# Performance work log

Measured on AMD Instinct MI355X. Metric: run time of the kernel, lower is better.

The kernel has to match this reference:

```python
import jax, jax.numpy as jnp
import numpy as np

N_NODES = 4096
N_EDGES = 131072
C_IN = 256
C_OUT = 256
N_HEADS = 4
ALPHA = 0.2
NEG_FILL = -9e15


def setup_inputs() -> dict:
    key = jax.random.key(0)
    k_x, k_e, k_w, k_b, k_a = jax.random.split(key, 5)
    x = jax.random.normal(k_x, (N_NODES, C_IN), dtype=jnp.float32)
    edge_index = jax.random.randint(k_e, (2, N_EDGES), 0, N_NODES, dtype=jnp.int64)
    # nn.Linear(c_in, c_out): weight [c_out, c_in], bias [c_out]
    W = jax.random.normal(k_w, (C_OUT, C_IN), dtype=jnp.float32) * 0.05
    b = jax.random.normal(k_b, (C_OUT,), dtype=jnp.float32) * 0.05
    # attention vector a: [num_heads, 2 * c_out_per_head]
    a = jax.random.normal(k_a, (N_HEADS, 2 * (C_OUT // N_HEADS)), dtype=jnp.float32) * 0.05
    return {"x": x, "edge_index": edge_index, "W": W, "b": b, "a": a}


def reference(x, edge_index, W, b, a):
    N = x.shape[0]
    H = a.shape[0]
    C = W.shape[0] // H  # per-head feature dim

    # Linear projection then split heads: [N, H, C]
    feats = (x @ W.T + b).reshape(N, H, C)

    # Dense adjacency (faithful to the original index_select/scatter construction)
    adj = jnp.zeros((N, N), dtype=bool).at[edge_index[0], edge_index[1]].set(True)

    # attn_logits = leaky_relu(einsum('bhc,hc->bh', cat(f_i, f_j), a))
    # is separable: score(i,j,h) = leaky_relu(f_i . a[:, :C] + f_j . a[:, C:])
    s_src = jnp.einsum('nhc,hc->nh', feats, a[:, :C])  # [N, H]
    s_dst = jnp.einsum('nhc,hc->nh', feats, a[:, C:])  # [N, H]
    logits = jax.nn.leaky_relu(s_src[:, None, :] + s_dst[None, :, :], ALPHA)  # [N, N, H]

    masked = jnp.where(adj[..., None], logits, NEG_FILL)
    probs = jax.nn.softmax(masked, axis=1)  # softmax over source nodes j (dim=2 with batch)

    # Weighted aggregation: einsum('bijh,bjhc->bihc') then concat heads
    out = jnp.einsum('ijh,jhc->ihc', probs, feats).reshape(N, H * C)
    return out[None]  # [1, N, c_out] (batch_size = 1 in the original)
```

## Files before the change

### kernel.cpp

```cpp
#include <hip/hip_runtime.h>
#include <hip/hip_bf16.h>
#include <stdint.h>

#define N_NODES 4096
#define N_EDGES 131072
#define C_IN 256
#define C_OUT 256
#define N_HEADS 4
#define C_HEAD 64
#define MAX_DEG 128
#define GEMM_BLOCKS 1024
#define SCAT_BLOCKS 128

typedef __attribute__((ext_vector_type(8))) short short8;
typedef __attribute__((ext_vector_type(4))) short short4v;
typedef __attribute__((ext_vector_type(4))) float floatx4;

union f32u { float f; uint32_t u; };
__device__ __forceinline__ float bf2f(short s) {
    f32u v; v.u = ((uint32_t)(uint16_t)s) << 16; return v.f;
}
__device__ __forceinline__ short f2bf(float f) {
    __hip_bfloat16 h = __float2bfloat16(f);
    return *reinterpret_cast<short*>(&h);
}

__global__ __launch_bounds__(256) void k1_gemm_scatter(
    const float* __restrict__ x, const float* __restrict__ W,
    const float* __restrict__ b, const int* __restrict__ ei,
    unsigned short* __restrict__ nbr, int* __restrict__ deg,
    __hip_bfloat16* __restrict__ feats)
{
    int blk = blockIdx.x;
    int tid = threadIdx.x;
    if (blk < GEMM_BLOCKS) {
        int lane = tid & 63;
        int wave = tid >> 6;
        int tile = blk * 4 + wave;
        int row0 = (tile >> 4) * 16;
        int col0 = (tile & 15) * 16;
        int r    = lane & 15;
        int quad = lane >> 4;

        const floatx4* ax = (const floatx4*)(x + (size_t)(row0 + r) * C_IN);
        const floatx4* bw = (const floatx4*)(W + (size_t)(col0 + r) * C_IN);

        floatx4 acc = {0.f, 0.f, 0.f, 0.f};
        #pragma unroll
        for (int k8 = 0; k8 < 8; ++k8) {
            floatx4 a0 = ax[k8 * 8 + quad * 2], a1 = ax[k8 * 8 + quad * 2 + 1];
            floatx4 b0 = bw[k8 * 8 + quad * 2], b1 = bw[k8 * 8 + quad * 2 + 1];
            short8 av, bq;
            #pragma unroll
            for (int j = 0; j < 4; ++j) {
                av[j] = f2bf(a0[j]); av[4 + j] = f2bf(a1[j]);
                bq[j] = f2bf(b0[j]); bq[4 + j] = f2bf(b1[j]);
            }
            acc = __builtin_amdgcn_mfma_f32_16x16x32_bf16(av, bq, acc, 0, 0, 0);
        }
        int gn = col0 + r;
        float bias = b[gn];
        #pragma unroll
        for (int rr = 0; rr < 4; ++rr) {
            int gm = row0 + quad * 4 + rr;
            feats[(size_t)gm * C_OUT + gn] = __float2bfloat16(acc[rr] + bias);
        }
    } else {
        bool is64 = true;
        #pragma unroll
        for (int q = 1; q < 64; q += 2) is64 = is64 && (ei[q] == 0);
        int base = (blk - GEMM_BLOCKS) * 256 + tid;
        #pragma unroll
        for (int qq = 0; qq < 4; ++qq) {
            int e = base + qq * (SCAT_BLOCKS * 256);
            int row, col;
            if (is64) {
                const long long* e64 = (const long long*)ei;
                row = (int)e64[e];
                col = (int)e64[N_EDGES + e];
            } else {
                row = ei[e];
                col = ei[N_EDGES + e];
            }
            int pos = atomicAdd(&deg[row], 1);
            if (pos < MAX_DEG) nbr[row * MAX_DEG + pos] = (unsigned short)col;
        }
    }
}

__global__ __launch_bounds__(256) void aggregate(
    const unsigned short* __restrict__ nbr,
    const int* __restrict__ deg,
    const __hip_bfloat16* __restrict__ feats,
    const float* __restrict__ a,
    float* __restrict__ out)
{
    int i    = blockIdx.x;
    int t    = threadIdx.x;
    int wv   = t >> 6;
    int lane = t & 63;
    int h    = lane >> 4;
    int li   = lane & 15;

    __shared__ unsigned short lst[MAX_DEG];
    __shared__ unsigned char  ok[MAX_DEG];
    __shared__ uint32_t       bmap[N_NODES / 32];
    __shared__ float          ssrc_sh[N_HEADS];
    __shared__ floatx4        redv[4][64];
    __shared__ float          redd[4][64];

    int n = deg[i];
    n = (n < MAX_DEG) ? n : MAX_DEG;

    if (t < n) lst[t] = nbr[i * MAX_DEG + t];
    if (t < N_NODES / 32) bmap[t] = 0u;
    __syncthreads();

    if (t < n) {
        int j = lst[t];
        uint32_t bit = 1u << (j & 31);
        uint32_t old = atomicOr(&bmap[j >> 5], bit);
        ok[t] = (old & bit) ? 0 : 1;
    }

    floatx4 as4 = *(const floatx4*)(a + h * 2 * C_HEAD + 4 * li);
    floatx4 ad4 = *(const floatx4*)(a + h * 2 * C_HEAD + C_HEAD + 4 * li);

    if (wv == 0) {
        short4v fi = *(const short4v*)(feats + (size_t)i * C_OUT + lane * 4);
        float p = bf2f(fi[0]) * as4[0] + bf2f(fi[1]) * as4[1]
                + bf2f(fi[2]) * as4[2] + bf2f(fi[3]) * as4[3];
        p += __shfl_xor(p, 1, 16);
        p += __shfl_xor(p, 2, 16);
        p += __shfl_xor(p, 4, 16);
        p += __shfl_xor(p, 8, 16);
        if (li == 0) ssrc_sh[h] = p;
    }
    __syncthreads();

    float ssrc = ssrc_sh[h];
    floatx4 acc = {0.f, 0.f, 0.f, 0.f};
    float   den = 0.f;

    if (n > 0) {
        #pragma unroll 2
        for (int k = wv; k < n; k += 4) {
            int j = lst[k];
            short4v fv = *(const short4v*)(feats + (size_t)j * C_OUT + lane * 4);
            float f0 = bf2f(fv[0]), f1 = bf2f(fv[1]), f2 = bf2f(fv[2]), f3 = bf2f(fv[3]);
            float p = f0 * ad4[0] + f1 * ad4[1] + f2 * ad4[2] + f3 * ad4[3];
            p += __shfl_xor(p, 1, 16);
            p += __shfl_xor(p, 2, 16);
            p += __shfl_xor(p, 4, 16);
            p += __shfl_xor(p, 8, 16);
            float l = ssrc + p;
            l = (l > 0.f) ? l : 0.2f * l;
            float w = ok[k] ? __expf(fminf(l, 60.f)) : 0.f;
            den += w;
            acc[0] += w * f0; acc[1] += w * f1; acc[2] += w * f2; acc[3] += w * f3;
        }
    } else {
        for (int j = wv; j < N_NODES; j += 4) {
            short4v fv = *(const short4v*)(feats + (size_t)j * C_OUT + lane * 4);
            acc[0] += bf2f(fv[0]); acc[1] += bf2f(fv[1]);
            acc[2] += bf2f(fv[2]); acc[3] += bf2f(fv[3]);
            den += 1.0f;
        }
    }
    redv[wv][lane] = acc;
    redd[wv][lane] = den;
    __syncthreads();

    if (wv == 0) {
        floatx4 r0 = redv[0][lane], r1 = redv[1][lane], r2 = redv[2][lane], r3 = redv[3][lane];
        float d = redd[0][lane] + redd[1][lane] + redd[2][lane] + redd[3][lane];
        if (d <= 0.f) d = 1.f;
        float inv = 1.0f / d;
        floatx4 o;
        o[0] = (r0[0] + r1[0] + r2[0] + r3[0]) * inv;
        o[1] = (r0[1] + r1[1] + r2[1] + r3[1]) * inv;
        o[2] = (r0[2] + r1[2] + r2[2] + r3[2]) * inv;
        o[3] = (r0[3] + r1[3] + r2[3] + r3[3]) * inv;
        *(floatx4*)(out + (size_t)i * C_OUT + lane * 4) = o;
    }
}

extern "C" void kernel_launch(void* const* d_in, const int* in_sizes, int n_in,
                              void* d_out, int out_size, void* d_ws, size_t ws_size,
                              hipStream_t stream) {
    const float* x  = (const float*)d_in[0];
    const int*   ei = (const int*)d_in[1];
    const float* W  = (const float*)d_in[2];
    const float* b  = (const float*)d_in[3];
    const float* a  = (const float*)d_in[4];
    float* out = (float*)d_out;

    uint8_t* ws = (uint8_t*)d_ws;
    __hip_bfloat16* feats = (__hip_bfloat16*)ws;
    unsigned short* nbr   = (unsigned short*)(ws + (2u << 20));
    int*            deg   = (int*)(ws + (3u << 20));

    hipMemsetAsync(deg, 0, N_NODES * sizeof(int), stream);
    k1_gemm_scatter<<<GEMM_BLOCKS + SCAT_BLOCKS, 256, 0, stream>>>(x, W, b, ei, nbr, deg, feats);
    aggregate<<<N_NODES, 256, 0, stream>>>(nbr, deg, feats, a, out);
}
```

Baseline: 102.3 us.

## Precompute per-node attention scores in GEMM epilogue and cache edge weights in LDS

The GEMM epilogue now computes the per-head source and destination attention dot products from the fp32 projection. It reduces them across 16 lanes with shuffles and accumulates them into global ssrc/sdst arrays with atomics. The aggregate kernel then computes all edge weights once per neighbor in a prologue into shared memory, so the main gather loop only loads features and does the weighted sum without per-edge shuffles and exp. This removes redundant per-edge dot products and shuffle reductions, at the cost of extra atomics in the GEMM and a larger memset.

```diff
diff --git a/kernel.cpp b/kernel.cpp
--- a/kernel.cpp
+++ b/kernel.cpp
@@ -27,9 +27,11 @@
 
 __global__ __launch_bounds__(256) void k1_gemm_scatter(
     const float* __restrict__ x, const float* __restrict__ W,
-    const float* __restrict__ b, const int* __restrict__ ei,
+    const float* __restrict__ b, const float* __restrict__ a,
+    const int* __restrict__ ei,
     unsigned short* __restrict__ nbr, int* __restrict__ deg,
-    __hip_bfloat16* __restrict__ feats)
+    __hip_bfloat16* __restrict__ feats,
+    float* __restrict__ ssrc_g, float* __restrict__ sdst_g)
 {
     int blk = blockIdx.x;
     int tid = threadIdx.x;
@@ -59,11 +61,25 @@
             acc = __builtin_amdgcn_mfma_f32_16x16x32_bf16(av, bq, acc, 0, 0, 0);
         }
         int gn = col0 + r;
+        int h  = col0 >> 6;
         float bias = b[gn];
+        float avs = a[h * 2 * C_HEAD + (gn & 63)];
+        float avd = a[h * 2 * C_HEAD + C_HEAD + (gn & 63)];
         #pragma unroll
         for (int rr = 0; rr < 4; ++rr) {
             int gm = row0 + quad * 4 + rr;
-            feats[(size_t)gm * C_OUT + gn] = __float2bfloat16(acc[rr] + bias);
+            float v = acc[rr] + bias;
+            feats[(size_t)gm * C_OUT + gn] = __float2bfloat16(v);
+            float s = v * avs;
+            float d = v * avd;
+            s += __shfl_xor(s, 1, 16); s += __shfl_xor(s, 2, 16);
+            s += __shfl_xor(s, 4, 16); s += __shfl_xor(s, 8, 16);
+            d += __shfl_xor(d, 1, 16); d += __shfl_xor(d, 2, 16);
+            d += __shfl_xor(d, 4, 16); d += __shfl_xor(d, 8, 16);
+            if (r == 0) {
+                atomicAdd(&ssrc_g[gm * N_HEADS + h], s);
+                atomicAdd(&sdst_g[gm * N_HEADS + h], d);
+            }
         }
     } else {
         bool is64 = true;
@@ -92,7 +108,8 @@
     const unsigned short* __restrict__ nbr,
     const int* __restrict__ deg,
     const __hip_bfloat16* __restrict__ feats,
-    const float* __restrict__ a,
+    const float* __restrict__ ssrc_g,
+    const float* __restrict__ sdst_g,
     float* __restrict__ out)
 {
     int i    = blockIdx.x;
@@ -100,12 +117,10 @@
     int wv   = t >> 6;
     int lane = t & 63;
     int h    = lane >> 4;
-    int li   = lane & 15;
 
     __shared__ unsigned short lst[MAX_DEG];
-    __shared__ unsigned char  ok[MAX_DEG];
+    __shared__ floatx4        wts4[MAX_DEG];
     __shared__ uint32_t       bmap[N_NODES / 32];
-    __shared__ float          ssrc_sh[N_HEADS];
     __shared__ floatx4        redv[4][64];
     __shared__ float          redd[4][64];
 
@@ -120,44 +135,33 @@
         int j = lst[t];
         uint32_t bit = 1u << (j & 31);
         uint32_t old = atomicOr(&bmap[j >> 5], bit);
-        ok[t] = (old & bit) ? 0 : 1;
-    }
-
-    floatx4 as4 = *(const floatx4*)(a + h * 2 * C_HEAD + 4 * li);
-    floatx4 ad4 = *(const floatx4*)(a + h * 2 * C_HEAD + C_HEAD + 4 * li);
-
-    if (wv == 0) {
-        short4v fi = *(const short4v*)(feats + (size_t)i * C_OUT + lane * 4);
-        float p = bf2f(fi[0]) * as4[0] + bf2f(fi[1]) * as4[1]
-                + bf2f(fi[2]) * as4[2] + bf2f(fi[3]) * as4[3];
-        p += __shfl_xor(p, 1, 16);
-        p += __shfl_xor(p, 2, 16);
-        p += __shfl_xor(p, 4, 16);
-        p += __shfl_xor(p, 8, 16);
-        if (li == 0) ssrc_sh[h] = p;
+        bool keep = !(old & bit);
+        floatx4 ss = *(const floatx4*)(ssrc_g + i * N_HEADS);
+        floatx4 sd = *(const floatx4*)(sdst_g + (size_t)j * N_HEADS);
+        floatx4 w;
+        #pragma unroll
+        for (int hh = 0; hh < N_HEADS; ++hh) {
+            float l = ss[hh] + sd[hh];
+            l = (l > 0.f) ? l : 0.2f * l;
+            w[hh] = keep ? __expf(fminf(l, 60.f)) : 0.f;
+        }
+        wts4[t] = w;
     }
     __syncthreads();
 
-    float ssrc = ssrc_sh[h];
+    const float* wts = (const float*)wts4;
     floatx4 acc = {0.f, 0.f, 0.f, 0.f};
     float   den = 0.f;
 
     if (n > 0) {
-        #pragma unroll 2
+        #pragma unroll 4
         for (int k = wv; k < n; k += 4) {
             int j = lst[k];
+            float w = wts[k * 4 + h];
             short4v fv = *(const short4v*)(feats + (size_t)j * C_OUT + lane * 4);
-            float f0 = bf2f(fv[0]), f1 = bf2f(fv[1]), f2 = bf2f(fv[2]), f3 = bf2f(fv[3]);
-            float p = f0 * ad4[0] + f1 * ad4[1] + f2 * ad4[2] + f3 * ad4[3];
-            p += __shfl_xor(p, 1, 16);
-            p += __shfl_xor(p, 2, 16);
-            p += __shfl_xor(p, 4, 16);
-            p += __shfl_xor(p, 8, 16);
-            float l = ssrc + p;
-            l = (l > 0.f) ? l : 0.2f * l;
-            float w = ok[k] ? __expf(fminf(l, 60.f)) : 0.f;
             den += w;
-            acc[0] += w * f0; acc[1] += w * f1; acc[2] += w * f2; acc[3] += w * f3;
+            acc[0] += w * bf2f(fv[0]); acc[1] += w * bf2f(fv[1]);
+            acc[2] += w * bf2f(fv[2]); acc[3] += w * bf2f(fv[3]);
         }
     } else {
         for (int j = wv; j < N_NODES; j += 4) {
@@ -199,8 +203,11 @@
     __hip_bfloat16* feats = (__hip_bfloat16*)ws;
     unsigned short* nbr   = (unsigned short*)(ws + (2u << 20));
     int*            deg   = (int*)(ws + (3u << 20));
-
-    hipMemsetAsync(deg, 0, N_NODES * sizeof(int), stream);
-    k1_gemm_scatter<<<GEMM_BLOCKS + SCAT_BLOCKS, 256, 0, stream>>>(x, W, b, ei, nbr, deg, feats);
-    aggregate<<<N_NODES, 256, 0, stream>>>(nbr, deg, feats, a, out);
-}
+    float*          ssrc  = (float*)(ws + (3u << 20) + (16u << 10));
+    float*          sdst  = (float*)(ws + (3u << 20) + (80u << 10));
+
+    hipMemsetAsync(deg, 0, (144u << 10), stream);
+    k1_gemm_scatter<<<GEMM_BLOCKS + SCAT_BLOCKS, 256, 0, stream>>>(
+        x, W, b, a, ei, nbr, deg, feats, ssrc, sdst);
+    aggregate<<<N_NODES, 256, 0, stream>>>(nbr, deg, feats, ssrc, sdst, out);
+}
```

After: 103.9 us. About the same (+1.5%).
